# Kernel tuning notes

Measured on AMD Instinct MI355X. Metric: run time of the kernel, lower is better.

The kernel has to match this reference:

```python
import jax, jax.numpy as jnp
import numpy as np

D_MODEL = 1024
IDX_DIM = 64
SEQ = 4096
D_STATE = 64
EXPAND = 1
HEADDIM = 32
D_CONV = 4
D_INNER = EXPAND * D_MODEL
NHEADS = D_INNER // HEADDIM
CONV_DIM = D_INNER + 2 * D_STATE
D_IN_PROJ = 2 * D_INNER + 2 * D_STATE + NHEADS  # z, xBC, dt


def setup_inputs() -> dict:
    key = jax.random.key(0)
    ks = jax.random.split(key, 8)
    def rn(k, shape, scale=1.0):
        return jax.random.normal(k, shape, jnp.float32) * scale
    return {
        "x": rn(ks[0], (SEQ, D_MODEL)),
        "W_in": rn(ks[1], (D_IN_PROJ, D_MODEL), D_MODEL ** -0.5),
        "conv_w": rn(ks[2], (CONV_DIM, D_CONV), D_CONV ** -0.5),
        "conv_b": jnp.zeros((CONV_DIM,), jnp.float32),
        "dt_bias": rn(ks[3], (NHEADS,)),
        "A_log": jnp.log(jnp.arange(1, NHEADS + 1, dtype=jnp.float32)),
        "D": jnp.ones((NHEADS,), jnp.float32),
        "norm_w": jnp.ones((D_INNER,), jnp.float32),
        "W_out": rn(ks[4], (D_MODEL, D_INNER), D_INNER ** -0.5),
        "W_q": rn(ks[5], (IDX_DIM, D_MODEL), D_MODEL ** -0.5),
        "W_k": rn(ks[6], (IDX_DIM, D_MODEL), D_MODEL ** -0.5),
    }


def _silu(v):
    return v * jax.nn.sigmoid(v)


def _mamba2(x, W_in, conv_w, conv_b, dt_bias, A_log, Dp, norm_w, W_out):
    L = x.shape[0]
    zxbcdt = x @ W_in.T  # [L, D_IN_PROJ]
    z, xBC, dt = jnp.split(zxbcdt, [D_INNER, D_INNER + CONV_DIM], axis=-1)
    # depthwise causal conv1d, kernel D_CONV
    xc = jax.lax.conv_general_dilated(
        xBC.T[None],               # [1, C, L]
        conv_w[:, None, :],        # [C, 1, K]
        (1,), [(D_CONV - 1, 0)], feature_group_count=CONV_DIM)[0].T
    xBC = _silu(xc + conv_b)
    xs, B, C = jnp.split(xBC, [D_INNER, D_INNER + D_STATE], axis=-1)
    xs = xs.reshape(L, NHEADS, HEADDIM)
    dt = jax.nn.softplus(dt + dt_bias)   # [L, H]
    A = -jnp.exp(A_log)                  # [H]

    def step(h, inp):
        x_t, B_t, C_t, dt_t = inp        # [H,P], [N], [N], [H]
        dA = jnp.exp(dt_t * A)           # [H]
        h = h * dA[:, None, None] + (dt_t[:, None] * x_t)[:, :, None] * B_t[None, None, :]
        return h, jnp.einsum('hpn,n->hp', h, C_t)

    h0 = jnp.zeros((NHEADS, HEADDIM, D_STATE), x.dtype)
    _, ys = jax.lax.scan(step, h0, (xs, B, C, dt))  # ys: [L, H, P]
    y = ys + Dp[None, :, None] * xs
    y = y.reshape(L, D_INNER)
    y = y * _silu(z)                                 # gated RMSNorm
    y = y * jax.lax.rsqrt(jnp.mean(y * y, axis=-1, keepdims=True) + 1e-5) * norm_w
    return y @ W_out.T


def reference(x, W_in, conv_w, conv_b, dt_bias, A_log, D, norm_w, W_out, W_q, W_k):
    L = x.shape[0]
    x_mamba = _mamba2(x, W_in, conv_w, conv_b, dt_bias, A_log, D, norm_w, W_out)
    q = x_mamba @ W_q.T                  # [L, IDX_DIM]
    k = x @ W_k.T                        # [L, IDX_DIM]
    scores = jnp.einsum('ti,si->ts', q, k) * (IDX_DIM ** -0.5)
    mask = jnp.tril(jnp.ones((L, L), dtype=bool))
    return jnp.where(mask, scores, -jnp.inf)
```

## Files before the change

### kernel.cpp

```cpp
#include <hip/hip_runtime.h>
#include <math.h>

#define L_SEQ 4096
#define DMODEL 1024
#define DINNER 1024
#define DSTATE 64
#define NH 32
#define HD 32
#define CONVD 1152
#define DPROJ2 2272
#define KOFF 2208
#define QC 128
#define NC 32

#define NEG_FILL (-1e30f)

typedef __attribute__((ext_vector_type(8))) short short8;
typedef __attribute__((ext_vector_type(4))) float f32x4;
typedef unsigned short u16;

__device__ __forceinline__ u16 f2bf(float f) {
  unsigned int u = __float_as_uint(f);
  unsigned int r = (u + 0x7fffu + ((u >> 16) & 1u)) >> 16;
  return (u16)r;
}
__device__ __forceinline__ float bf2f(u16 b) {
  unsigned int u = ((unsigned int)b) << 16;
  return __uint_as_float(u);
}
__device__ __forceinline__ short8 pack8(float4 a, float4 b) {
  short8 v;
  v[0] = (short)f2bf(a.x); v[1] = (short)f2bf(a.y);
  v[2] = (short)f2bf(a.z); v[3] = (short)f2bf(a.w);
  v[4] = (short)f2bf(b.x); v[5] = (short)f2bf(b.y);
  v[6] = (short)f2bf(b.z); v[7] = (short)f2bf(b.w);
  return v;
}

__device__ __forceinline__ void g2l16(const void* g, void* l) {
  __builtin_amdgcn_global_load_lds(
      (const __attribute__((address_space(1))) unsigned int*)g,
      (__attribute__((address_space(3))) unsigned int*)l, 16, 0, 0);
}

__global__ __launch_bounds__(256) void cast_bf16_k(const float* __restrict__ in,
                                                   u16* __restrict__ out, int n) {
  int i = (blockIdx.x * 256 + threadIdx.x) * 8;
  if (i >= n) return;
  float4 f0 = *(const float4*)(in + i);
  float4 f1 = *(const float4*)(in + i + 4);
  *(short8*)(out + i) = pack8(f0, f1);
}

__global__ __launch_bounds__(256) void transpose_cast_k(const float* __restrict__ in,
                                                        u16* __restrict__ out) {
  __shared__ float tile[64][65];
  int tx = threadIdx.x & 63, ty = threadIdx.x >> 6;
  int bx = blockIdx.x, by = blockIdx.y;
#pragma unroll
  for (int k = 0; k < 16; k++) {
    int r = ty + k * 4;
    tile[r][tx] = in[(size_t)(by * 64 + r) * 1024 + bx * 64 + tx];
  }
  __syncthreads();
#pragma unroll
  for (int k = 0; k < 16; k++) {
    int r = ty + k * 4;
    out[(size_t)(bx * 64 + r) * 1024 + by * 64 + tx] = f2bf(tile[tx][r]);
  }
}

__global__ __launch_bounds__(256) void wqo_k(const u16* __restrict__ Wq,
                                             const u16* __restrict__ WoutT,
                                             u16* __restrict__ Wqo) {
  const int tid = threadIdx.x;
  const int wave = tid >> 6, lane = tid & 63;
  const int l15 = lane & 15, quad = lane >> 4;
  const int j0 = blockIdx.x * 64;
  f32x4 acc[4] = {};
  for (int kk = 0; kk < 32; kk++) {
    short8 b = *(const short8*)(WoutT + (size_t)(j0 + wave * 16 + l15) * 1024 + kk * 32 + quad * 8);
#pragma unroll
    for (int mi = 0; mi < 4; mi++) {
      short8 a = *(const short8*)(Wq + (size_t)(mi * 16 + l15) * 1024 + kk * 32 + quad * 8);
      acc[mi] = __builtin_amdgcn_mfma_f32_16x16x32_bf16(a, b, acc[mi], 0, 0, 0);
    }
  }
#pragma unroll
  for (int mi = 0; mi < 4; mi++)
#pragma unroll
    for (int r = 0; r < 4; r++) {
      int i = mi * 16 + quad * 4 + r;
      Wqo[(size_t)i * 1024 + j0 + wave * 16 + l15] = f2bf(acc[mi][r]);
    }
}

__global__ __launch_bounds__(256) void gemm_n64(const u16* __restrict__ A,
                                                const u16* __restrict__ B,
                                                u16* __restrict__ Cbf,
                                                int M, int N, int K) {
  __shared__ u16 As[128 * 32];
  __shared__ u16 Bs[64 * 32];
  const int tid = threadIdx.x;
  const int wave = tid >> 6, lane = tid & 63;
  const int m0 = blockIdx.x * 128, n0 = blockIdx.y * 64;
  const int wm = (wave >> 1) * 64, wn = (wave & 1) * 32;
  const int l15 = lane & 15, quad = lane >> 4;

  const int c0 = tid, c1 = 256 + tid;
  const int r0 = c0 >> 2, q0 = (c0 & 3) ^ ((r0 >> 1) & 3);
  const int r1 = c1 >> 2, q1 = (c1 & 3) ^ ((r1 >> 1) & 3);
  const int rb = tid >> 2, qb = (tid & 3) ^ ((rb >> 1) & 3);
  const u16* a0 = A + (size_t)(m0 + r0) * K + q0 * 8;
  const u16* a1 = A + (size_t)(m0 + r1) * K + q1 * 8;
  const int bn = min(n0 + rb, N - 1);
  const u16* bptr = B + (size_t)bn * K + qb * 8;
  char* ldsA0 = (char*)As + wave * 1024;
  char* ldsA1 = (char*)As + 4096 + wave * 1024;
  char* ldsB = (char*)Bs + wave * 1024;

  int offA[4], offB[2];
#pragma unroll
  for (int i = 0; i < 4; i++) {
    int ra = wm + i * 16 + l15;
    offA[i] = ra * 32 + (quad ^ ((ra >> 1) & 3)) * 8;
  }
#pragma unroll
  for (int j = 0; j < 2; j++) {
    int rr = wn + j * 16 + l15;
    offB[j] = rr * 32 + (quad ^ ((rr >> 1) & 3)) * 8;
  }

  f32x4 acc[4][2] = {};
  for (int k0 = 0; k0 < K; k0 += 32) {
    g2l16(a0 + k0, ldsA0);
    g2l16(a1 + k0, ldsA1);
    g2l16(bptr + k0, ldsB);
    __builtin_amdgcn_s_waitcnt(0);
    __syncthreads();
    short8 af[4], bfr[2];
#pragma unroll
    for (int i = 0; i < 4; i++) af[i] = *(const short8*)(As + offA[i]);
#pragma unroll
    for (int j = 0; j < 2; j++) bfr[j] = *(const short8*)(Bs + offB[j]);
#pragma unroll
    for (int mi = 0; mi < 4; mi++)
#pragma unroll
      for (int ni = 0; ni < 2; ni++)
        acc[mi][ni] = __builtin_amdgcn_mfma_f32_16x16x32_bf16(af[mi], bfr[ni],
                                                              acc[mi][ni], 0, 0, 0);
    __syncthreads();
  }
#pragma unroll
  for (int mi = 0; mi < 4; mi++)
#pragma unroll
    for (int r = 0; r < 4; r++) {
      int grow = m0 + wm + mi * 16 + quad * 4 + r;
#pragma unroll
      for (int ni = 0; ni < 2; ni++) {
        int gcol = n0 + wn + ni * 16 + l15;
        if (gcol < N) Cbf[(size_t)grow * N + gcol] = f2bf(acc[mi][ni][r]);
      }
    }
}

__global__ __launch_bounds__(256) void splitk64(const u16* __restrict__ A,
                                                const u16* __restrict__ B,
                                                float* __restrict__ P,
                                                int M, int K) {
  __shared__ u16 As[128 * 32];
  __shared__ u16 Bs[64 * 32];
  const int tid = threadIdx.x;
  const int wave = tid >> 6, lane = tid & 63;
  const int m0 = blockIdx.x * 128;
  const int ks = blockIdx.y;
  const int wm = (wave >> 1) * 64, wn = (wave & 1) * 32;
  const int l15 = lane & 15, quad = lane >> 4;

  const int c0 = tid, c1 = 256 + tid;
  const int r0 = c0 >> 2, q0 = (c0 & 3) ^ ((r0 >> 1) & 3);
  const int r1 = c1 >> 2, q1 = (c1 & 3) ^ ((r1 >> 1) & 3);
  const int rb = tid >> 2, qb = (tid & 3) ^ ((rb >> 1) & 3);
  const u16* a0 = A + (size_t)(m0 + r0) * K + q0 * 8;
  const u16* a1 = A + (size_t)(m0 + r1) * K + q1 * 8;
  const u16* bptr = B + (size_t)rb * K + qb * 8;
  char* ldsA0 = (char*)As + wave * 1024;
  char* ldsA1 = (char*)As + 4096 + wave * 1024;
  char* ldsB = (char*)Bs + wave * 1024;

  int offA[4], offB[2];
#pragma unroll
  for (int i = 0; i < 4; i++) {
    int ra = wm + i * 16 + l15;
    offA[i] = ra * 32 + (quad ^ ((ra >> 1) & 3)) * 8;
  }
#pragma unroll
  for (int j = 0; j < 2; j++) {
    int rr = wn + j * 16 + l15;
    offB[j] = rr * 32 + (quad ^ ((rr >> 1) & 3)) * 8;
  }

  f32x4 acc[4][2] = {};
  const int kbeg = ks * 128;
  for (int k0 = kbeg; k0 < kbeg + 128; k0 += 32) {
    g2l16(a0 + k0, ldsA0);
    g2l16(a1 + k0, ldsA1);
    g2l16(bptr + k0, ldsB);
    __builtin_amdgcn_s_waitcnt(0);
    __syncthreads();
    short8 af[4], bfr[2];
#pragma unroll
    for (int i = 0; i < 4; i++) af[i] = *(const short8*)(As + offA[i]);
#pragma unroll
    for (int j = 0; j < 2; j++) bfr[j] = *(const short8*)(Bs + offB[j]);
#pragma unroll
    for (int mi = 0; mi < 4; mi++)
#pragma unroll
      for (int ni = 0; ni < 2; ni++)
        acc[mi][ni] = __builtin_amdgcn_mfma_f32_16x16x32_bf16(af[mi], bfr[ni],
                                                              acc[mi][ni], 0, 0, 0);
    __syncthreads();
  }
  float* Pp = P + (size_t)ks * M * 64;
#pragma unroll
  for (int mi = 0; mi < 4; mi++)
#pragma unroll
    for (int r = 0; r < 4; r++) {
      int grow = m0 + wm + mi * 16 + quad * 4 + r;
#pragma unroll
      for (int ni = 0; ni < 2; ni++)
        Pp[(size_t)grow * 64 + wn + ni * 16 + l15] = acc[mi][ni][r];
    }
}

__global__ __launch_bounds__(256) void reduce8_k(const float* __restrict__ P,
                                                 u16* __restrict__ out, int n) {
  int i = blockIdx.x * 256 + threadIdx.x;
  if (i >= n) return;
  float s = 0.f;
#pragma unroll
  for (int ks = 0; ks < 8; ks++) s += P[(size_t)ks * n + i];
  out[i] = f2bf(s);
}

__global__ __launch_bounds__(256) void conv_silu_k(const u16* __restrict__ zx,
                                                   const float* __restrict__ cw,
                                                   const float* __restrict__ cb,
                                                   u16* __restrict__ xbc) {
  int c0 = threadIdx.x * 8;
  int t = blockIdx.x;
  if (c0 >= CONVD) return;
  float acc[8];
#pragma unroll
  for (int j = 0; j < 8; j++) acc[j] = cb[c0 + j];
  float wv[8][4];
#pragma unroll
  for (int j = 0; j < 8; j++) {
    float4 w4 = *(const float4*)(cw + (c0 + j) * 4);
    wv[j][0] = w4.x; wv[j][1] = w4.y; wv[j][2] = w4.z; wv[j][3] = w4.w;
  }
#pragma unroll
  for (int k = 0; k < 4; k++) {
    int s = t - 3 + k;
    if (s >= 0) {
      short8 v = *(const short8*)(zx + (size_t)s * DPROJ2 + DINNER + c0);
#pragma unroll
      for (int j = 0; j < 8; j++) acc[j] += bf2f((u16)v[j]) * wv[j][k];
    }
  }
  short8 o;
#pragma unroll
  for (int j = 0; j < 8; j++) o[j] = (short)f2bf(acc[j] / (1.f + expf(-acc[j])));
  *(short8*)(xbc + (size_t)t * CONVD + c0) = o;
}

__global__ void dtcum_k(const u16* __restrict__ zx,
                        const float* __restrict__ dt_bias,
                        const float* __restrict__ A_log,
                        float* __restrict__ dtsp,
                        float* __restrict__ aL) {
  int h = blockIdx.x & 31, c = blockIdx.x >> 5;
  int lane = threadIdx.x;
  float negA = -expf(A_log[h]);
  float bias = dt_bias[h];
  float carry = 0.f;
#pragma unroll
  for (int seg = 0; seg < 2; seg++) {
    int t = c * QC + seg * 64 + lane;
    float xv = bf2f(zx[(size_t)t * DPROJ2 + 2176 + h]) + bias;
    float sp = (xv > 20.f) ? xv : log1pf(expf(xv));
    dtsp[(size_t)t * 32 + h] = sp;
    float v = sp * negA;
#pragma unroll
    for (int off = 1; off < 64; off <<= 1) {
      float u = __shfl_up(v, off, 64);
      if (lane >= off) v += u;
    }
    aL[(size_t)t * 32 + h] = carry + v;
    carry += __shfl(v, 63, 64);
  }
}

__global__ __launch_bounds__(256) void chunk_state_mfma(const u16* __restrict__ xbc,
                                                        const float* __restrict__ dtsp,
                                                        const float* __restrict__ aL,
                                                        float* __restrict__ S) {
  int h = blockIdx.x & 31, c = blockIdx.x >> 5;
  int tid = threadIdx.x;
  __shared__ __align__(16) u16 sXs[32 * 136];
  __shared__ __align__(16) u16 sBT[64 * 136];
  __shared__ float scoef[QC];
  if (tid < QC) {
    float aend = aL[(size_t)(c * QC + QC - 1) * 32 + h];
    float a = aL[(size_t)(c * QC + tid) * 32 + h];
    scoef[tid] = expf(aend - a) * dtsp[(size_t)(c * QC + tid) * 32 + h];
  }
  __syncthreads();
  for (int j = tid; j < 32 * QC / 8; j += 256) {
    int s = j & 127, p0 = (j >> 7) * 8;
    short8 v = *(const short8*)(xbc + (size_t)(c * QC + s) * CONVD + h * HD + p0);
    float cf = scoef[s];
#pragma unroll
    for (int e = 0; e < 8; e++) sXs[(p0 + e) * 136 + s] = f2bf(cf * bf2f((u16)v[e]));
  }
  for (int j = tid; j < 64 * QC / 8; j += 256) {
    int s = j & 127, n0 = (j >> 7) * 8;
    short8 v = *(const short8*)(xbc + (size_t)(c * QC + s) * CONVD + DINNER + n0);
#pragma unroll
    for (int e = 0; e < 8; e++) sBT[(n0 + e) * 136 + s] = (u16)v[e];
  }
  __syncthreads();
  const int wave = tid >> 6, lane = tid & 63;
  const int l15 = lane & 15, quad = lane >> 4;
  f32x4 acc[2] = {};
#pragma unroll
  for (int kk = 0; kk < 4; kk++) {
    short8 b = *(const short8*)(sBT + (wave * 16 + l15) * 136 + kk * 32 + quad * 8);
#pragma unroll
    for (int i = 0; i < 2; i++) {
      short8 a = *(const short8*)(sXs + (i * 16 + l15) * 136 + kk * 32 + quad * 8);
      acc[i] = __builtin_amdgcn_mfma_f32_16x16x32_bf16(a, b, acc[i], 0, 0, 0);
    }
  }
  float* Sb = S + ((size_t)c * 32 + h) * 2048;
#pragma unroll
  for (int i = 0; i < 2; i++)
#pragma unroll
    for (int r = 0; r < 4; r++) {
      int p = i * 16 + quad * 4 + r;
      Sb[p * 64 + wave * 16 + l15] = acc[i][r];
    }
}

__global__ __launch_bounds__(256) void state_scan_k(const float* __restrict__ S,
                                                    const float* __restrict__ aL,
                                                    float* __restrict__ Hinit) {
  int idx = blockIdx.x * 256 + threadIdx.x;
  int h = idx >> 11, rem = idx & 2047;
  float E = 0.f;
#pragma unroll
  for (int c = 0; c < NC; c++) {
    size_t o = ((size_t)c * 32 + h) * 2048 + rem;
    Hinit[o] = E;
    float dec = expf(aL[(size_t)(c * QC + QC - 1) * 32 + h]);
    E = E * dec + S[o];
  }
}

__global__ __launch_bounds__(256) void gmat_mfma(const u16* __restrict__ xbc,
                                                 float* __restrict__ G) {
  int c = blockIdx.x;
  int tid = threadIdx.x;
  const int wave = tid >> 6, lane = tid & 63;
  const int wm = (wave >> 1) * 64, wn = (wave & 1) * 64;
  const int l15 = lane & 15, quad = lane >> 4;
  f32x4 acc[4][4] = {};
#pragma unroll
  for (int kk = 0; kk < 2; kk++) {
    short8 a[4], b[4];
#pragma unroll
    for (int i = 0; i < 4; i++) {
      int t = wm + i * 16 + l15;
      a[i] = *(const short8*)(xbc + (size_t)(c * QC + t) * CONVD + DINNER + DSTATE + kk * 32 + quad * 8);
      int s = wn + i * 16 + l15;
      b[i] = *(const short8*)(xbc + (size_t)(c * QC + s) * CONVD + DINNER + kk * 32 + quad * 8);
    }
#pragma unroll
    for (int mi = 0; mi < 4; mi++)
#pragma unroll
      for (int ni = 0; ni < 4; ni++)
        acc[mi][ni] = __builtin_amdgcn_mfma_f32_16x16x32_bf16(a[mi], b[ni],
                                                              acc[mi][ni], 0, 0, 0);
  }
  float* Gb = G + (size_t)c * QC * QC;
#pragma unroll
  for (int mi = 0; mi < 4; mi++)
#pragma unroll
    for (int r = 0; r < 4; r++) {
      int t = wm + mi * 16 + quad * 4 + r;
#pragma unroll
      for (int ni = 0; ni < 4; ni++)
        Gb[(size_t)t * QC + wn + ni * 16 + l15] = acc[mi][ni][r];
    }
}

__global__ __launch_bounds__(256) void yout_mfma(const u16* __restrict__ xbc,
                                                 const float* __restrict__ dtsp,
                                                 const float* __restrict__ aL,
                                                 const float* __restrict__ G,
                                                 const float* __restrict__ Hinit,
                                                 const float* __restrict__ Dv,
                                                 u16* __restrict__ y) {
  int h = blockIdx.x & 31, c = blockIdx.x >> 5;
  int tid = threadIdx.x;
  __shared__ __align__(16) u16 sXT[32 * 136];
  __shared__ float sa[QC];
  __shared__ float sd[QC];

  if (tid < QC) {
    sa[tid] = aL[(size_t)(c * QC + tid) * 32 + h];
    sd[tid] = dtsp[(size_t)(c * QC + tid) * 32 + h];
  }
  for (int j = tid; j < 32 * QC / 8; j += 256) {
    int t = j & 127, p0 = (j >> 7) * 8;
    short8 v = *(const short8*)(xbc + (size_t)(c * QC + t) * CONVD + h * HD + p0);
#pragma unroll
    for (int e = 0; e < 8; e++) sXT[(p0 + e) * 136 + t] = (u16)v[e];
  }
  __syncthreads();

  const int wave = tid >> 6, lane = tid & 63;
  const int l15 = lane & 15, quad = lane >> 4;
  f32x4 acc1[2][2] = {};
  f32x4 acc2[2][2] = {};

#pragma unroll
  for (int kk = 0; kk < 4; kk++) {
    short8 b[2];
#pragma unroll
    for (int j = 0; j < 2; j++)
      b[j] = *(const short8*)(sXT + (j * 16 + l15) * 136 + kk * 32 + quad * 8);
#pragma unroll
    for (int i = 0; i < 2; i++) {
      int rmax = wave * 32 + i * 16 + 15;
      if (kk * 32 > rmax) continue;
      int m = wave * 32 + i * 16 + l15;
      float am = sa[m];
      const float* Gp = G + (size_t)c * QC * QC + (size_t)m * QC + kk * 32 + quad * 8;
      float4 g0 = *(const float4*)Gp;
      float4 g1 = *(const float4*)(Gp + 4);
      float gv[8] = {g0.x, g0.y, g0.z, g0.w, g1.x, g1.y, g1.z, g1.w};
      int s0 = kk * 32 + quad * 8;
      short8 a;
#pragma unroll
      for (int j2 = 0; j2 < 8; j2++) {
        int s = s0 + j2;
        float w = 0.f;
        if (s <= m) w = expf(am - sa[s]) * sd[s] * gv[j2];
        a[j2] = (short)f2bf(w);
      }
#pragma unroll
      for (int j = 0; j < 2; j++)
        acc1[i][j] = __builtin_amdgcn_mfma_f32_16x16x32_bf16(a, b[j], acc1[i][j], 0, 0, 0);
    }
  }

  const float* Hbase = Hinit + ((size_t)c * 32 + h) * 2048;
#pragma unroll
  for (int kk = 0; kk < 2; kk++) {
    short8 b[2];
#pragma unroll
    for (int j = 0; j < 2; j++) {
      const float* Hp = Hbase + (size_t)(j * 16 + l15) * 64 + kk * 32 + quad * 8;
      b[j] = pack8(*(const float4*)Hp, *(const float4*)(Hp + 4));
    }
#pragma unroll
    for (int i = 0; i < 2; i++) {
      int t = wave * 32 + i * 16 + l15;
      short8 a = *(const short8*)(xbc + (size_t)(c * QC + t) * CONVD + DINNER + DSTATE + kk * 32 + quad * 8);
#pragma unroll
      for (int j = 0; j < 2; j++)
        acc2[i][j] = __builtin_amdgcn_mfma_f32_16x16x32_bf16(a, b[j], acc2[i][j], 0, 0, 0);
    }
  }

  float Dh = Dv[h];
#pragma unroll
  for (int i = 0; i < 2; i++) {
#pragma unroll
    for (int r = 0; r < 4; r++) {
      int t = wave * 32 + i * 16 + quad * 4 + r;
      float et = expf(sa[t]);
#pragma unroll
      for (int j = 0; j < 2; j++) {
        int p = j * 16 + l15;
        float xv = bf2f(sXT[p * 136 + t]);
        float val = acc1[i][j][r] + et * acc2[i][j][r] + Dh * xv;
        y[(size_t)(c * QC + t) * DINNER + h * HD + p] = f2bf(val);
      }
    }
  }
}

__global__ __launch_bounds__(256) void rmsnorm_k(const u16* __restrict__ y1,
                                                 const u16* __restrict__ zx,
                                                 const float* __restrict__ nw,
                                                 u16* __restrict__ y2) {
  int t = blockIdx.x, tid = threadIdx.x;
  int d0 = tid * 4;
  ushort4 yv = *(const ushort4*)(y1 + (size_t)t * DINNER + d0);
  ushort4 zv = *(const ushort4*)(zx + (size_t)t * DPROJ2 + d0);
  float v[4];
  float ss = 0.f;
  u16 ya[4] = {yv.x, yv.y, yv.z, yv.w};
  u16 za[4] = {zv.x, zv.y, zv.z, zv.w};
#pragma unroll
  for (int i = 0; i < 4; i++) {
    float z = bf2f(za[i]);
    float val = bf2f(ya[i]) * (z / (1.f + expf(-z)));
    v[i] = val;
    ss += val * val;
  }
#pragma unroll
  for (int off = 32; off > 0; off >>= 1) ss += __shfl_xor(ss, off, 64);
  __shared__ float red[4];
  int wid = tid >> 6, lane = tid & 63;
  if (lane == 0) red[wid] = ss;
  __syncthreads();
  ss = red[0] + red[1] + red[2] + red[3];
  float scale = rsqrtf(ss * (1.f / 1024.f) + 1e-5f);
  float4 w4 = *(const float4*)(nw + d0);
  float wa[4] = {w4.x, w4.y, w4.z, w4.w};
  ushort4 o;
  o.x = f2bf(v[0] * scale * wa[0]);
  o.y = f2bf(v[1] * scale * wa[1]);
  o.z = f2bf(v[2] * scale * wa[2]);
  o.w = f2bf(v[3] * scale * wa[3]);
  *(ushort4*)(y2 + (size_t)t * DINNER + d0) = o;
}

__global__ __launch_bounds__(256) void scores_mfma(const u16* __restrict__ q,
                                                   const u16* __restrict__ kmat,
                                                   int kstride,
                                                   float* __restrict__ out) {
  const int m0 = blockIdx.y * 128, n0 = blockIdx.x * 128;
  const int tid = threadIdx.x;
  if (n0 > m0 + 127) {
    float4 f = make_float4(NEG_FILL, NEG_FILL, NEG_FILL, NEG_FILL);
    for (int i = tid; i < 128 * 32; i += 256) {
      int row = i >> 5, c4 = (i & 31) << 2;
      *(float4*)(out + (size_t)(m0 + row) * L_SEQ + n0 + c4) = f;
    }
    return;
  }
  const int wave = tid >> 6, lane = tid & 63;
  const int wm = (wave >> 1) * 64, wn = (wave & 1) * 64;
  const int l15 = lane & 15, quad = lane >> 4;
  f32x4 acc[4][4] = {};
#pragma unroll
  for (int kk = 0; kk < 2; kk++) {
    short8 a[4], b[4];
#pragma unroll
    for (int i = 0; i < 4; i++) {
      a[i] = *(const short8*)(q + (size_t)(m0 + wm + i * 16 + l15) * 64 + kk * 32 + quad * 8);
      b[i] = *(const short8*)(kmat + (size_t)(n0 + wn + i * 16 + l15) * kstride + kk * 32 + quad * 8);
    }
#pragma unroll
    for (int mi = 0; mi < 4; mi++)
#pragma unroll
      for (int ni = 0; ni < 4; ni++)
        acc[mi][ni] = __builtin_amdgcn_mfma_f32_16x16x32_bf16(a[mi], b[ni],
                                                              acc[mi][ni], 0, 0, 0);
  }
#pragma unroll
  for (int mi = 0; mi < 4; mi++)
#pragma unroll
    for (int r = 0; r < 4; r++) {
      int row = m0 + wm + mi * 16 + quad * 4 + r;
#pragma unroll
      for (int ni = 0; ni < 4; ni++) {
        int col = n0 + wn + ni * 16 + l15;
        out[(size_t)row * L_SEQ + col] = (col <= row) ? acc[mi][ni][r] * 0.125f : NEG_FILL;
      }
    }
}

extern "C" void kernel_launch(void* const* d_in, const int* in_sizes, int n_in,
                              void* d_out, int out_size, void* d_ws, size_t ws_size,
                              hipStream_t stream) {
  const float* x       = (const float*)d_in[0];
  const float* W_in    = (const float*)d_in[1];
  const float* conv_w  = (const float*)d_in[2];
  const float* conv_b  = (const float*)d_in[3];
  const float* dt_bias = (const float*)d_in[4];
  const float* A_log   = (const float*)d_in[5];
  const float* Dv      = (const float*)d_in[6];
  const float* norm_w  = (const float*)d_in[7];
  const float* W_out   = (const float*)d_in[8];
  const float* W_q     = (const float*)d_in[9];
  const float* W_k     = (const float*)d_in[10];
  float* out = (float*)d_out;

  char* ws = (char*)d_ws;
  size_t off = 0;
  auto alloc = [&](size_t bytes) {
    void* p = (void*)(ws + off);
    off += (bytes + 255) & ~(size_t)255;
    return p;
  };
  u16* zx_bf    = (u16*)alloc((size_t)L_SEQ * DPROJ2 * 2);
  u16* xbc_bf   = (u16*)alloc((size_t)L_SEQ * CONVD * 2);
  float* dtsp   = (float*)alloc((size_t)L_SEQ * NH * 4);
  float* aL     = (float*)alloc((size_t)L_SEQ * NH * 4);
  float* S      = (float*)alloc((size_t)NC * NH * HD * DSTATE * 4);
  float* Hinit  = (float*)alloc((size_t)NC * NH * HD * DSTATE * 4);
  float* G      = (float*)alloc((size_t)NC * QC * QC * 4);
  u16* y1_bf    = (u16*)alloc((size_t)L_SEQ * DINNER * 2);
  u16* y2_bf    = (u16*)alloc((size_t)L_SEQ * DINNER * 2);
  u16* x_bf     = (u16*)alloc((size_t)L_SEQ * DMODEL * 2);
  u16* Wcat_bf  = (u16*)alloc((size_t)DPROJ2 * DMODEL * 2);
  u16* WoutT_bf = (u16*)alloc((size_t)DMODEL * DINNER * 2);
  u16* Wq_bf    = (u16*)alloc((size_t)64 * DMODEL * 2);
  u16* Wqo_bf   = (u16*)alloc((size_t)64 * DINNER * 2);
  u16* q_bf     = (u16*)alloc((size_t)L_SEQ * 64 * 2);
  float* Pq = S;

  cast_bf16_k<<<dim3(L_SEQ * DMODEL / 2048), 256, 0, stream>>>(x, x_bf, L_SEQ * DMODEL);
  cast_bf16_k<<<dim3(2208 * DMODEL / 2048), 256, 0, stream>>>(W_in, Wcat_bf, 2208 * DMODEL);
  cast_bf16_k<<<dim3(64 * DMODEL / 2048), 256, 0, stream>>>(W_k, Wcat_bf + (size_t)2208 * DMODEL, 64 * DMODEL);
  cast_bf16_k<<<dim3(64 * DMODEL / 2048), 256, 0, stream>>>(W_q, Wq_bf, 64 * DMODEL);
  transpose_cast_k<<<dim3(16, 16), 256, 0, stream>>>(W_out, WoutT_bf);
  wqo_k<<<dim3(16), 256, 0, stream>>>(Wq_bf, WoutT_bf, Wqo_bf);
  gemm_n64<<<dim3(L_SEQ / 128, (DPROJ2 + 63) / 64), 256, 0, stream>>>(
      x_bf, Wcat_bf, zx_bf, L_SEQ, DPROJ2, DMODEL);
  conv_silu_k<<<dim3(L_SEQ), 256, 0, stream>>>(zx_bf, conv_w, conv_b, xbc_bf);
  dtcum_k<<<dim3(NC * NH), 64, 0, stream>>>(zx_bf, dt_bias, A_log, dtsp, aL);
  chunk_state_mfma<<<dim3(NC * NH), 256, 0, stream>>>(xbc_bf, dtsp, aL, S);
  state_scan_k<<<dim3(NH * HD * DSTATE / 256), 256, 0, stream>>>(S, aL, Hinit);
  gmat_mfma<<<dim3(NC), 256, 0, stream>>>(xbc_bf, G);
  yout_mfma<<<dim3(NC * NH), 256, 0, stream>>>(xbc_bf, dtsp, aL, G, Hinit, Dv, y1_bf);
  rmsnorm_k<<<dim3(L_SEQ), 256, 0, stream>>>(y1_bf, zx_bf, norm_w, y2_bf);
  splitk64<<<dim3(L_SEQ / 128, 8), 256, 0, stream>>>(y2_bf, Wqo_bf, Pq, L_SEQ, DINNER);
  reduce8_k<<<dim3(L_SEQ * 64 / 256), 256, 0, stream>>>(Pq, q_bf, L_SEQ * 64);
  scores_mfma<<<dim3(32, 32), 256, 0, stream>>>(q_bf, zx_bf + KOFF, DPROJ2, out);
}
```

Measured before the change: 262.8 us.

## Fuse cast launches, deepen GEMM K tile, repack conv threads, nontemporal score stores

Merges the four fp32-to-bf16 cast launches into one kernel that picks its source by global thread index. The input-projection GEMM now stages a K-tile of 64 with a wider XOR swizzle, halving the barrier and wait count per K. The conv kernel maps threads densely (144 per timestep) so no lanes idle. The score output now uses nontemporal stores to avoid polluting cache with the large fp32 output. These trade some extra LDS use and index arithmetic for fewer launches, fewer synchronisations and better write behaviour.

```diff
diff --git a/kernel.cpp b/kernel.cpp
--- a/kernel.cpp
+++ b/kernel.cpp
@@ -43,13 +43,30 @@
       (__attribute__((address_space(3))) unsigned int*)l, 16, 0, 0);
 }
 
-__global__ __launch_bounds__(256) void cast_bf16_k(const float* __restrict__ in,
-                                                   u16* __restrict__ out, int n) {
-  int i = (blockIdx.x * 256 + threadIdx.x) * 8;
-  if (i >= n) return;
-  float4 f0 = *(const float4*)(in + i);
-  float4 f1 = *(const float4*)(in + i + 4);
-  *(short8*)(out + i) = pack8(f0, f1);
+#define CAST_N0 (L_SEQ * DMODEL / 8)
+#define CAST_N1 (2208 * DMODEL / 8)
+#define CAST_N2 (64 * DMODEL / 8)
+#define CAST_TOTAL (CAST_N0 + CAST_N1 + 2 * CAST_N2)
+__global__ __launch_bounds__(256) void cast_all_k(const float* __restrict__ x,
+                                                  const float* __restrict__ W_in,
+                                                  const float* __restrict__ W_k,
+                                                  const float* __restrict__ W_q,
+                                                  u16* __restrict__ x_bf,
+                                                  u16* __restrict__ Wcat,
+                                                  u16* __restrict__ Wq_bf) {
+  int gid = blockIdx.x * 256 + threadIdx.x;
+  const float* src;
+  u16* dst;
+  int i;
+  if (gid < CAST_N0) { src = x; dst = x_bf; i = gid; }
+  else if (gid < CAST_N0 + CAST_N1) { src = W_in; dst = Wcat; i = gid - CAST_N0; }
+  else if (gid < CAST_N0 + CAST_N1 + CAST_N2) {
+    src = W_k; dst = Wcat + (size_t)2208 * DMODEL; i = gid - CAST_N0 - CAST_N1;
+  } else { src = W_q; dst = Wq_bf; i = gid - CAST_N0 - CAST_N1 - CAST_N2; }
+  i *= 8;
+  float4 f0 = *(const float4*)(src + i);
+  float4 f1 = *(const float4*)(src + i + 4);
+  *(short8*)(dst + i) = pack8(f0, f1);
 }
 
 __global__ __launch_bounds__(256) void transpose_cast_k(const float* __restrict__ in,
@@ -99,56 +116,71 @@
                                                 const u16* __restrict__ B,
                                                 u16* __restrict__ Cbf,
                                                 int M, int N, int K) {
-  __shared__ u16 As[128 * 32];
-  __shared__ u16 Bs[64 * 32];
+  __shared__ u16 As[128 * 64];
+  __shared__ u16 Bs[64 * 64];
   const int tid = threadIdx.x;
   const int wave = tid >> 6, lane = tid & 63;
   const int m0 = blockIdx.x * 128, n0 = blockIdx.y * 64;
   const int wm = (wave >> 1) * 64, wn = (wave & 1) * 32;
   const int l15 = lane & 15, quad = lane >> 4;
 
-  const int c0 = tid, c1 = 256 + tid;
-  const int r0 = c0 >> 2, q0 = (c0 & 3) ^ ((r0 >> 1) & 3);
-  const int r1 = c1 >> 2, q1 = (c1 & 3) ^ ((r1 >> 1) & 3);
-  const int rb = tid >> 2, qb = (tid & 3) ^ ((rb >> 1) & 3);
-  const u16* a0 = A + (size_t)(m0 + r0) * K + q0 * 8;
-  const u16* a1 = A + (size_t)(m0 + r1) * K + q1 * 8;
-  const int bn = min(n0 + rb, N - 1);
-  const u16* bptr = B + (size_t)bn * K + qb * 8;
-  char* ldsA0 = (char*)As + wave * 1024;
-  char* ldsA1 = (char*)As + 4096 + wave * 1024;
-  char* ldsB = (char*)Bs + wave * 1024;
-
-  int offA[4], offB[2];
-#pragma unroll
-  for (int i = 0; i < 4; i++) {
-    int ra = wm + i * 16 + l15;
-    offA[i] = ra * 32 + (quad ^ ((ra >> 1) & 3)) * 8;
-  }
-#pragma unroll
-  for (int j = 0; j < 2; j++) {
-    int rr = wn + j * 16 + l15;
-    offB[j] = rr * 32 + (quad ^ ((rr >> 1) & 3)) * 8;
+  const u16* aptr[4];
+  const u16* bptr[2];
+  char* ldsA[4];
+  char* ldsB[2];
+#pragma unroll
+  for (int b = 0; b < 4; b++) {
+    int ch = b * 256 + tid;
+    int row = ch >> 3, q = (ch & 7) ^ (row & 7);
+    aptr[b] = A + (size_t)(m0 + row) * K + q * 8;
+    ldsA[b] = (char*)As + b * 4096 + wave * 1024;
+  }
+#pragma unroll
+  for (int b = 0; b < 2; b++) {
+    int ch = b * 256 + tid;
+    int row = ch >> 3, q = (ch & 7) ^ (row & 7);
+    int bn = min(n0 + row, N - 1);
+    bptr[b] = B + (size_t)bn * K + q * 8;
+    ldsB[b] = (char*)Bs + b * 4096 + wave * 1024;
+  }
+
+  int offA[2][4], offB[2][2];
+#pragma unroll
+  for (int kk = 0; kk < 2; kk++) {
+#pragma unroll
+    for (int i = 0; i < 4; i++) {
+      int r = wm + i * 16 + l15;
+      offA[kk][i] = r * 64 + ((kk * 4 + quad) ^ (r & 7)) * 8;
+    }
+#pragma unroll
+    for (int j = 0; j < 2; j++) {
+      int r = wn + j * 16 + l15;
+      offB[kk][j] = r * 64 + ((kk * 4 + quad) ^ (r & 7)) * 8;
+    }
   }
 
   f32x4 acc[4][2] = {};
-  for (int k0 = 0; k0 < K; k0 += 32) {
-    g2l16(a0 + k0, ldsA0);
-    g2l16(a1 + k0, ldsA1);
-    g2l16(bptr + k0, ldsB);
+  for (int k0 = 0; k0 < K; k0 += 64) {
+#pragma unroll
+    for (int b = 0; b < 4; b++) g2l16(aptr[b] + k0, ldsA[b]);
+#pragma unroll
+    for (int b = 0; b < 2; b++) g2l16(bptr[b] + k0, ldsB[b]);
     __builtin_amdgcn_s_waitcnt(0);
     __syncthreads();
-    short8 af[4], bfr[2];
-#pragma unroll
-    for (int i = 0; i < 4; i++) af[i] = *(const short8*)(As + offA[i]);
-#pragma unroll
-    for (int j = 0; j < 2; j++) bfr[j] = *(const short8*)(Bs + offB[j]);
-#pragma unroll
-    for (int mi = 0; mi < 4; mi++)
-#pragma unroll
-      for (int ni = 0; ni < 2; ni++)
-        acc[mi][ni] = __builtin_amdgcn_mfma_f32_16x16x32_bf16(af[mi], bfr[ni],
-                                                              acc[mi][ni], 0, 0, 0);
+#pragma unroll
+    for (int kk = 0; kk < 2; kk++) {
+      short8 af[4], bfr[2];
+#pragma unroll
+      for (int i = 0; i < 4; i++) af[i] = *(const short8*)(As + offA[kk][i]);
+#pragma unroll
+      for (int j = 0; j < 2; j++) bfr[j] = *(const short8*)(Bs + offB[kk][j]);
+#pragma unroll
+      for (int mi = 0; mi < 4; mi++)
+#pragma unroll
+        for (int ni = 0; ni < 2; ni++)
+          acc[mi][ni] = __builtin_amdgcn_mfma_f32_16x16x32_bf16(af[mi], bfr[ni],
+                                                                acc[mi][ni], 0, 0, 0);
+    }
     __syncthreads();
   }
 #pragma unroll
@@ -247,9 +279,9 @@
                                                    const float* __restrict__ cw,
                                                    const float* __restrict__ cb,
                                                    u16* __restrict__ xbc) {
-  int c0 = threadIdx.x * 8;
-  int t = blockIdx.x;
-  if (c0 >= CONVD) return;
+  int gid = blockIdx.x * 256 + threadIdx.x;
+  int t = gid / 144;
+  int c0 = (gid - t * 144) * 8;
   float acc[8];
 #pragma unroll
   for (int j = 0; j < 8; j++) acc[j] = cb[c0 + j];
@@ -546,10 +578,10 @@
   const int m0 = blockIdx.y * 128, n0 = blockIdx.x * 128;
   const int tid = threadIdx.x;
   if (n0 > m0 + 127) {
-    float4 f = make_float4(NEG_FILL, NEG_FILL, NEG_FILL, NEG_FILL);
+    f32x4 f = {NEG_FILL, NEG_FILL, NEG_FILL, NEG_FILL};
     for (int i = tid; i < 128 * 32; i += 256) {
       int row = i >> 5, c4 = (i & 31) << 2;
-      *(float4*)(out + (size_t)(m0 + row) * L_SEQ + n0 + c4) = f;
+      __builtin_nontemporal_store(f, (f32x4*)(out + (size_t)(m0 + row) * L_SEQ + n0 + c4));
     }
     return;
   }
@@ -580,7 +612,8 @@
 #pragma unroll
       for (int ni = 0; ni < 4; ni++) {
         int col = n0 + wn + ni * 16 + l15;
-        out[(size_t)row * L_SEQ + col] = (col <= row) ? acc[mi][ni][r] * 0.125f : NEG_FILL;
+        float val = (col <= row) ? acc[mi][ni][r] * 0.125f : NEG_FILL;
+        __builtin_nontemporal_store(val, out + (size_t)row * L_SEQ + col);
       }
     }
 }
@@ -625,15 +658,13 @@
   u16* q_bf     = (u16*)alloc((size_t)L_SEQ * 64 * 2);
   float* Pq = S;
 
-  cast_bf16_k<<<dim3(L_SEQ * DMODEL / 2048), 256, 0, stream>>>(x, x_bf, L_SEQ * DMODEL);
-  cast_bf16_k<<<dim3(2208 * DMODEL / 2048), 256, 0, stream>>>(W_in, Wcat_bf, 2208 * DMODEL);
-  cast_bf16_k<<<dim3(64 * DMODEL / 2048), 256, 0, stream>>>(W_k, Wcat_bf + (size_t)2208 * DMODEL, 64 * DMODEL);
-  cast_bf16_k<<<dim3(64 * DMODEL / 2048), 256, 0, stream>>>(W_q, Wq_bf, 64 * DMODEL);
+  cast_all_k<<<dim3(CAST_TOTAL / 256), 256, 0, stream>>>(x, W_in, W_k, W_q,
+                                                         x_bf, Wcat_bf, Wq_bf);
   transpose_cast_k<<<dim3(16, 16), 256, 0, stream>>>(W_out, WoutT_bf);
   wqo_k<<<dim3(16), 256, 0, stream>>>(Wq_bf, WoutT_bf, Wqo_bf);
   gemm_n64<<<dim3(L_SEQ / 128, (DPROJ2 + 63) / 64), 256, 0, stream>>>(
       x_bf, Wcat_bf, zx_bf, L_SEQ, DPROJ2, DMODEL);
-  conv_silu_k<<<dim3(L_SEQ), 256, 0, stream>>>(zx_bf, conv_w, conv_b, xbc_bf);
+  conv_silu_k<<<dim3(L_SEQ * 144 / 256), 256, 0, stream>>>(zx_bf, conv_w, conv_b, xbc_bf);
   dtcum_k<<<dim3(NC * NH), 64, 0, stream>>>(zx_bf, dt_bias, A_log, dtsp, aL);
   chunk_state_mfma<<<dim3(NC * NH), 256, 0, stream>>>(xbc_bf, dtsp, aL, S);
   state_scan_k<<<dim3(NH * HD * DSTATE / 256), 256, 0, stream>>>(S, aL, Hinit);
```

Measured after the change: 247.7 us. -5.8%, faster.
